# Performance work log

Measured on AMD Instinct MI355X. Metric: run time of the kernel, lower is better.

Reference implementation:

```python
import jax, jax.numpy as jnp
import numpy as np

K = 64          # tagset size (len(tag_to_ix))
START = 62      # start_tag_id
STOP = 63       # stop_tag_id
NEG = -10000.0


def setup_inputs() -> dict:
    key = jax.random.key(0)
    k1, k2, k3 = jax.random.split(key, 3)
    B, T = 1024, 512
    feats = jax.random.normal(k1, (B, T, K), dtype=jnp.float32)
    tags = jax.random.randint(k2, (B, T), 0, K, dtype=jnp.int32)
    # learned transition matrix; transitions[i, j] = score of moving from tag j to tag i
    transitions = jax.random.normal(k3, (K, K), dtype=jnp.float32)
    transitions = transitions.at[START, :].set(NEG).at[:, STOP].set(NEG)
    return {"feats": feats, "tags": tags, "transitions": transitions}


def reference(feats, tags, transitions):
    B, T, _ = feats.shape
    # log_alpha init: -10000 everywhere except start tag (matches torch code; feats[:,0] unused)
    alpha0 = jnp.full((B, K), NEG, dtype=feats.dtype).at[:, START].set(0.0)

    def step(alpha, feat_t):
        # alpha: [B, K]; new_alpha[b, i] = lse_j(transitions[i, j] + alpha[b, j]) + feat_t[b, i]
        new_alpha = jax.nn.logsumexp(transitions[None, :, :] + alpha[:, None, :], axis=-1) + feat_t
        return new_alpha, None

    feats_seq = jnp.transpose(feats[:, 1:, :], (1, 0, 2))  # [T-1, B, K]
    alpha, _ = jax.lax.scan(step, alpha0, feats_seq)
    forward_score = jax.nn.logsumexp(alpha, axis=-1)  # [B]

    # gold path score: sum_t transitions[tags[t], tags[t-1]] + feats[t, tags[t]], t = 1..T-1
    trans_score = transitions[tags[:, 1:], tags[:, :-1]].sum(axis=1)  # [B]
    emit_score = jnp.take_along_axis(feats[:, 1:, :], tags[:, 1:, None], axis=2)[..., 0].sum(axis=1)  # [B]
    gold_score = trans_score + emit_score

    return jnp.mean(forward_score - gold_score)
```

## Files before the change

kernel.cpp:

```cpp
#include <hip/hip_runtime.h>


#define BB 1024
#define TT 512
#define KK 64
#define GB 16
#define NJ 15
#define SEGLEN 32
#define LN2F 0.6931471805599453f

typedef _Float16 f16;
typedef f16   f16x8 __attribute__((ext_vector_type(8)));
typedef float f32x4 __attribute__((ext_vector_type(4)));

union W8 { f16x8 v; f16 e[8]; };

#define MFMA16(A, B, C) __builtin_amdgcn_mfma_f32_16x16x32_f16((A), (B), (C), 0, 0, 0)

__device__ __forceinline__ f32x4 exp4(f32x4 u) {
  f32x4 r; r.x = __expf(u.x); r.y = __expf(u.y); r.z = __expf(u.z); r.w = __expf(u.w);
  return r;
}

__device__ __forceinline__ unsigned umaxu(unsigned a, unsigned b) { return a > b ? a : b; }

__device__ __forceinline__ void normalize(const f32x4 (&q)[4], f32x4 (&v)[4], int& esum) {
  unsigned t0 = umaxu(umaxu(__float_as_uint(q[0].x), __float_as_uint(q[0].y)),
                      umaxu(__float_as_uint(q[0].z), __float_as_uint(q[0].w)));
  unsigned t1 = umaxu(umaxu(__float_as_uint(q[1].x), __float_as_uint(q[1].y)),
                      umaxu(__float_as_uint(q[1].z), __float_as_uint(q[1].w)));
  unsigned t2 = umaxu(umaxu(__float_as_uint(q[2].x), __float_as_uint(q[2].y)),
                      umaxu(__float_as_uint(q[2].z), __float_as_uint(q[2].w)));
  unsigned t3 = umaxu(umaxu(__float_as_uint(q[3].x), __float_as_uint(q[3].y)),
                      umaxu(__float_as_uint(q[3].z), __float_as_uint(q[3].w)));
  unsigned mb = umaxu(umaxu(t0, t1), umaxu(t2, t3));
  mb = umaxu(mb, (unsigned)__shfl_xor((int)mb, 16));
  mb = umaxu(mb, (unsigned)__shfl_xor((int)mb, 32));
  esum += (int)(mb >> 23) - 127;
  const float s = __uint_as_float(0x7F000000u - (mb & 0x7F800000u));
  #pragma unroll
  for (int tau = 0; tau < 4; ++tau) v[tau] = q[tau] * s;
}

__device__ __forceinline__ void pack_w(const f32x4 (&v)[4], W8 (&whi)[2], W8 (&wlo)[2]) {
  #pragma unroll
  for (int S = 0; S < 2; ++S) {
    #pragma unroll
    for (int c = 0; c < 2; ++c) {
      const f32x4 t = v[2 * S + c];
      const f16 h0 = (f16)t.x, h1 = (f16)t.y, h2 = (f16)t.z, h3 = (f16)t.w;
      whi[S].e[4 * c + 0] = h0;
      whi[S].e[4 * c + 1] = h1;
      whi[S].e[4 * c + 2] = h2;
      whi[S].e[4 * c + 3] = h3;
      wlo[S].e[4 * c + 0] = (f16)(t.x - (float)h0);
      wlo[S].e[4 * c + 1] = (f16)(t.y - (float)h1);
      wlo[S].e[4 * c + 2] = (f16)(t.z - (float)h2);
      wlo[S].e[4 * c + 3] = (f16)(t.w - (float)h3);
    }
  }
}

__device__ __forceinline__ void mfma_step(const W8 (&Ehi)[4][2], const W8 (&Elo)[4][2],
                                          const W8 (&whi)[2], const W8 (&wlo)[2],
                                          f32x4 (&acc)[4]) {
  #pragma unroll
  for (int tau = 0; tau < 4; ++tau) {
    f32x4 a = {0.f, 0.f, 0.f, 0.f};
    a = MFMA16(Ehi[tau][0].v, whi[0].v, a);
    a = MFMA16(Ehi[tau][1].v, whi[1].v, a);
    a = MFMA16(Elo[tau][0].v, whi[0].v, a);
    a = MFMA16(Elo[tau][1].v, whi[1].v, a);
    a = MFMA16(Ehi[tau][0].v, wlo[0].v, a);
    a = MFMA16(Ehi[tau][1].v, wlo[1].v, a);
    acc[tau] = a;
  }
}

template <int DIR, int D>
__device__ __forceinline__ void step_one(
    const float* __restrict__ fB, int j, int t_lo, int t_hi,
    const W8 (&Ehi)[4][2], const W8 (&Elo)[4][2],
    W8 (&whi)[2], W8 (&wlo)[2],
    f32x4 (&uR)[4][4], f32x4 (&g)[4],
    f32x4 (&v)[4], int& esum)
{
  f32x4 acc[4];
  mfma_step(Ehi, Elo, whi, wlo, acc);

  int tn = DIR ? (t_hi - 1 - (j + 4)) : (t_lo + (j + 4));
  if (DIR) { if (tn < t_lo) tn = t_lo; } else { if (tn > t_hi) tn = t_hi; }
  #pragma unroll
  for (int tau = 0; tau < 4; ++tau)
    uR[D][tau] = *(const f32x4*)(fB + (size_t)tn * KK + 16 * tau);

  f32x4 q[4];
  #pragma unroll
  for (int tau = 0; tau < 4; ++tau) q[tau] = acc[tau] * g[tau];
  normalize(q, v, esum);
  pack_w(v, whi, wlo);

  constexpr int DN = (D + 1) & 3;
  #pragma unroll
  for (int tau = 0; tau < 4; ++tau) g[tau] = exp4(uR[DN][tau]);
}

template <int DIR>
__device__ __forceinline__ void run_seg(
    const float* __restrict__ feats, const float* __restrict__ trans,
    int grp, int lane, int t_lo, int t_hi, int nstep, int one_hot,
    f32x4 (&v)[4], int& esum)
{
  const int m = lane & 15;
  const int h = lane >> 4;

  W8 Ehi[4][2], Elo[4][2];
  #pragma unroll
  for (int tau = 0; tau < 4; ++tau)
    #pragma unroll
    for (int S = 0; S < 2; ++S)
      #pragma unroll
      for (int e = 0; e < 8; ++e) {
        const int kk = 32 * S + 16 * (e >> 2) + 4 * h + (e & 3);
        const int row = 16 * tau + m;
        const float val = __expf(DIR ? trans[kk * KK + row] : trans[row * KK + kk]);
        const f16 hi = (f16)val;
        Ehi[tau][S].e[e] = hi;
        Elo[tau][S].e[e] = (f16)(val - (float)hi);
      }

  const float* fB = feats + (size_t)(grp * GB + m) * TT * KK + 4 * h;

  f32x4 uR[4][4];
  #pragma unroll
  for (int d = 0; d < 4; ++d) {
    int t = DIR ? (t_hi - 1 - d) : (t_lo + d);
    if (DIR) { if (t < t_lo) t = t_lo; } else { if (t > t_hi) t = t_hi; }
    #pragma unroll
    for (int tau = 0; tau < 4; ++tau)
      uR[d][tau] = *(const f32x4*)(fB + (size_t)t * KK + 16 * tau);
  }

  W8 whi[2], wlo[2];
  f32x4 g[4];
  esum = 0;

  if (DIR == 0) {
    f32x4 vv[4];
    if (one_hot) {
      #pragma unroll
      for (int tau = 0; tau < 4; ++tau) vv[tau] = (f32x4){0.f, 0.f, 0.f, 0.f};
      if (h == 3) vv[3].z = 1.0f;
    } else {
      #pragma unroll
      for (int tau = 0; tau < 4; ++tau) vv[tau] = (f32x4){1.f, 1.f, 1.f, 1.f};
    }
    pack_w(vv, whi, wlo);
  } else {
    f32x4 q[4];
    #pragma unroll
    for (int tau = 0; tau < 4; ++tau)
      q[tau] = exp4(*(const f32x4*)(fB + (size_t)t_hi * KK + 16 * tau));
    normalize(q, v, esum);
    pack_w(v, whi, wlo);
  }
  #pragma unroll
  for (int tau = 0; tau < 4; ++tau) g[tau] = exp4(uR[0][tau]);

  const int nq = nstep >> 2;
  for (int gg = 0; gg < nq; ++gg) {
    const int j = 4 * gg;
    step_one<DIR, 0>(fB, j + 0, t_lo, t_hi, Ehi, Elo, whi, wlo, uR, g, v, esum);
    step_one<DIR, 1>(fB, j + 1, t_lo, t_hi, Ehi, Elo, whi, wlo, uR, g, v, esum);
    step_one<DIR, 2>(fB, j + 2, t_lo, t_hi, Ehi, Elo, whi, wlo, uR, g, v, esum);
    step_one<DIR, 3>(fB, j + 3, t_lo, t_hi, Ehi, Elo, whi, wlo, uR, g, v, esum);
  }
  const int jr = 4 * nq;
  const int rem = nstep & 3;
  if (rem > 0) step_one<DIR, 0>(fB, jr + 0, t_lo, t_hi, Ehi, Elo, whi, wlo, uR, g, v, esum);
  if (rem > 1) step_one<DIR, 1>(fB, jr + 1, t_lo, t_hi, Ehi, Elo, whi, wlo, uR, g, v, esum);
  if (rem > 2) step_one<DIR, 2>(fB, jr + 2, t_lo, t_hi, Ehi, Elo, whi, wlo, uR, g, v, esum);

  if (DIR == 1) {
    f32x4 acc[4];
    mfma_step(Ehi, Elo, whi, wlo, acc);
    normalize(acc, v, esum);
  }
}

__global__ void zero_diff_kernel(float* __restrict__ diff) {
  diff[threadIdx.x] = 0.0f;
}

__global__ __launch_bounds__(128, 1) void crf_seg_kernel(
    const float* __restrict__ feats,
    const int*   __restrict__ tags,
    const float* __restrict__ trans,
    float*       __restrict__ diff)
{
  __shared__ float ysh[KK][GB];
  __shared__ int   esum_sh[GB];
  __shared__ float gpart[GB];

  const int chainBlocks = 64 * NJ;

  if ((int)blockIdx.x < chainBlocks) {
    const int lane = threadIdx.x & 63;
    const int wv   = threadIdx.x >> 6;
    const int grp  = blockIdx.x / NJ;
    const int j    = 1 + blockIdx.x % NJ;
    const int m = lane & 15;
    const int h = lane >> 4;

    f32x4 v[4];
    int esum;

    if (wv == 1) {
      const int t_lo = SEGLEN * j + 1;
      const int t_hi = (j == NJ) ? (TT - 1) : SEGLEN * (j + 1);
      run_seg<1>(feats, trans, grp, lane, t_lo, t_hi, t_hi - t_lo, 0, v, esum);
      #pragma unroll
      for (int tau = 0; tau < 4; ++tau) {
        ysh[16 * tau + 4 * h + 0][m] = v[tau].x;
        ysh[16 * tau + 4 * h + 1][m] = v[tau].y;
        ysh[16 * tau + 4 * h + 2][m] = v[tau].z;
        ysh[16 * tau + 4 * h + 3][m] = v[tau].w;
      }
      if (lane < 16) esum_sh[lane] = esum;
      __syncthreads();
    } else {
      const int t_lo = SEGLEN * (j - 1) + 1;
      const int t_hi = SEGLEN * j;
      run_seg<0>(feats, trans, grp, lane, t_lo, t_hi, SEGLEN, j == 1, v, esum);

      __syncthreads();

      float A = 0.f, Bs = 0.f;
      #pragma unroll
      for (int tau = 0; tau < 4; ++tau) {
        A += v[tau].x * ysh[16 * tau + 4 * h + 0][m];
        A += v[tau].y * ysh[16 * tau + 4 * h + 1][m];
        A += v[tau].z * ysh[16 * tau + 4 * h + 2][m];
        A += v[tau].w * ysh[16 * tau + 4 * h + 3][m];
        Bs += (v[tau].x + v[tau].y) + (v[tau].z + v[tau].w);
      }
      A  += __shfl_xor(A, 16);  A  += __shfl_xor(A, 32);
      Bs += __shfl_xor(Bs, 16); Bs += __shfl_xor(Bs, 32);

      if (lane < 16) {
        float c = __logf(A) + (float)(esum + esum_sh[lane]) * LN2F;
        if (j > 1) c -= __logf(Bs) + (float)esum * LN2F;
        atomicAdd(&diff[grp * GB + lane], c);
      }
    }
  } else {
    const int grp = blockIdx.x - chainBlocks;
    const int tid = threadIdx.x;
    const int m   = tid & 15;
    const int h8  = tid >> 4;
    const int bglob = grp * GB + m;
    const int* tg = tags + bglob * TT;
    const float* fg = feats + (size_t)bglob * TT * KK;

    float gs = 0.f;
    #pragma unroll 8
    for (int tt = 1 + h8; tt < TT; tt += 8) {
      const int tc = tg[tt];
      const int tp = tg[tt - 1];
      gs += trans[tc * KK + tp] + fg[(size_t)tt * KK + tc];
    }
    gs += __shfl_xor(gs, 16);
    gs += __shfl_xor(gs, 32);
    if (tid >= 64 && (tid & 63) < 16) gpart[tid & 15] = gs;
    __syncthreads();
    if (tid < 16) atomicAdd(&diff[grp * GB + tid], -(gs + gpart[tid]));
  }
}

__global__ __launch_bounds__(1024) void reduce_mean_kernel(
    const float* __restrict__ diff, float* __restrict__ out)
{
  __shared__ float part[16];
  const int tid = threadIdx.x;
  float v = diff[tid];
  #pragma unroll
  for (int off = 32; off; off >>= 1) v += __shfl_xor(v, off);
  if ((tid & 63) == 0) part[tid >> 6] = v;
  __syncthreads();
  if (tid < 16) {
    float s = part[tid];
    #pragma unroll
    for (int off = 8; off; off >>= 1) s += __shfl_xor(s, off);
    if (tid == 0) out[0] = s * (1.0f / 1024.0f);
  }
}

extern "C" void kernel_launch(void* const* d_in, const int* in_sizes, int n_in,
                              void* d_out, int out_size, void* d_ws, size_t ws_size,
                              hipStream_t stream) {
  const float* feats = (const float*)d_in[0];
  const int*   tags  = (const int*)d_in[1];
  const float* trans = (const float*)d_in[2];
  float* out  = (float*)d_out;
  float* diff = (float*)d_ws;

  zero_diff_kernel<<<dim3(1), dim3(1024), 0, stream>>>(diff);
  crf_seg_kernel<<<dim3(64 * NJ + 64), dim3(128), 0, stream>>>(feats, tags, trans, diff);
  reduce_mean_kernel<<<dim3(1), dim3(1024), 0, stream>>>(diff, out);
}
```

Baseline: 228.3 us.

## Halve segment length, precompute exp-transition MFMA fragments in a prep kernel

Splits the sequence into 31 segments of 16 steps instead of 15 of 32, doubling the number of chain blocks so the serial recurrence per block is shorter and more blocks run in parallel. The hi/lo fp16 fragments of exp(transitions) are now built once by a separate prep kernel and loaded per lane, instead of every block evaluating 64 exps per lane. Launch bounds allow up to 4 blocks per CU. This adds an extra kernel launch and more segment-combination work in exchange for a shorter critical path.

```diff
diff --git a/kernel.cpp b/kernel.cpp
--- a/kernel.cpp
+++ b/kernel.cpp
@@ -5,15 +5,15 @@
 #define TT 512
 #define KK 64
 #define GB 16
-#define NJ 15
-#define SEGLEN 32
+#define NJ 31
+#define SEGLEN 16
 #define LN2F 0.6931471805599453f
 
 typedef _Float16 f16;
 typedef f16   f16x8 __attribute__((ext_vector_type(8)));
 typedef float f32x4 __attribute__((ext_vector_type(4)));
 
-union W8 { f16x8 v; f16 e[8]; };
+union W8 { f16x8 v; f16 e[8]; uint4 u; };
 
 #define MFMA16(A, B, C) __builtin_amdgcn_mfma_f32_16x16x32_f16((A), (B), (C), 0, 0, 0)
 
@@ -107,10 +107,93 @@
 
 template <int DIR>
 __device__ __forceinline__ void run_seg(
-    const float* __restrict__ feats, const float* __restrict__ trans,
+    const float* __restrict__ feats, const uint4* __restrict__ frags,
     int grp, int lane, int t_lo, int t_hi, int nstep, int one_hot,
     f32x4 (&v)[4], int& esum)
 {
+  const int m = lane & 15;
+  const int h = lane >> 4;
+
+  W8 Ehi[4][2], Elo[4][2];
+  {
+    const uint4* fr = frags + DIR * 1024 + lane;
+    #pragma unroll
+    for (int tau = 0; tau < 4; ++tau)
+      #pragma unroll
+      for (int S = 0; S < 2; ++S) {
+        Ehi[tau][S].u = fr[(tau * 2 + S) * 64];
+        Elo[tau][S].u = fr[(8 + tau * 2 + S) * 64];
+      }
+  }
+
+  const float* fB = feats + (size_t)(grp * GB + m) * TT * KK + 4 * h;
+
+  f32x4 uR[4][4];
+  #pragma unroll
+  for (int d = 0; d < 4; ++d) {
+    int t = DIR ? (t_hi - 1 - d) : (t_lo + d);
+    if (DIR) { if (t < t_lo) t = t_lo; } else { if (t > t_hi) t = t_hi; }
+    #pragma unroll
+    for (int tau = 0; tau < 4; ++tau)
+      uR[d][tau] = *(const f32x4*)(fB + (size_t)t * KK + 16 * tau);
+  }
+
+  W8 whi[2], wlo[2];
+  f32x4 g[4];
+  esum = 0;
+
+  if (DIR == 0) {
+    f32x4 vv[4];
+    if (one_hot) {
+      #pragma unroll
+      for (int tau = 0; tau < 4; ++tau) vv[tau] = (f32x4){0.f, 0.f, 0.f, 0.f};
+      if (h == 3) vv[3].z = 1.0f;
+    } else {
+      #pragma unroll
+      for (int tau = 0; tau < 4; ++tau) vv[tau] = (f32x4){1.f, 1.f, 1.f, 1.f};
+    }
+    pack_w(vv, whi, wlo);
+  } else {
+    f32x4 q[4];
+    #pragma unroll
+    for (int tau = 0; tau < 4; ++tau)
+      q[tau] = exp4(*(const f32x4*)(fB + (size_t)t_hi * KK + 16 * tau));
+    normalize(q, v, esum);
+    pack_w(v, whi, wlo);
+  }
+  #pragma unroll
+  for (int tau = 0; tau < 4; ++tau) g[tau] = exp4(uR[0][tau]);
+
+  const int nq = nstep >> 2;
+  for (int gg = 0; gg < nq; ++gg) {
+    const int j = 4 * gg;
+    step_one<DIR, 0>(fB, j + 0, t_lo, t_hi, Ehi, Elo, whi, wlo, uR, g, v, esum);
+    step_one<DIR, 1>(fB, j + 1, t_lo, t_hi, Ehi, Elo, whi, wlo, uR, g, v, esum);
+    step_one<DIR, 2>(fB, j + 2, t_lo, t_hi, Ehi, Elo, whi, wlo, uR, g, v, esum);
+    step_one<DIR, 3>(fB, j + 3, t_lo, t_hi, Ehi, Elo, whi, wlo, uR, g, v, esum);
+  }
+  const int jr = 4 * nq;
+  const int rem = nstep & 3;
+  if (rem > 0) step_one<DIR, 0>(fB, jr + 0, t_lo, t_hi, Ehi, Elo, whi, wlo, uR, g, v, esum);
+  if (rem > 1) step_one<DIR, 1>(fB, jr + 1, t_lo, t_hi, Ehi, Elo, whi, wlo, uR, g, v, esum);
+  if (rem > 2) step_one<DIR, 2>(fB, jr + 2, t_lo, t_hi, Ehi, Elo, whi, wlo, uR, g, v, esum);
+
+  if (DIR == 1) {
+    f32x4 acc[4];
+    mfma_step(Ehi, Elo, whi, wlo, acc);
+    normalize(acc, v, esum);
+  }
+}
+
+__global__ void zero_diff_kernel(float* __restrict__ diff) {
+  diff[threadIdx.x] = 0.0f;
+}
+
+__global__ __launch_bounds__(128) void prep_kernel(
+    const float* __restrict__ trans, uint4* __restrict__ frags)
+{
+  const int lane = threadIdx.x & 63;
+  const int DIR  = threadIdx.x >> 6;
   const int m = lane & 15;
   const int h = lane >> 4;
 
@@ -129,73 +212,21 @@
         Elo[tau][S].e[e] = (f16)(val - (float)hi);
       }
 
-  const float* fB = feats + (size_t)(grp * GB + m) * TT * KK + 4 * h;
-
-  f32x4 uR[4][4];
-  #pragma unroll
-  for (int d = 0; d < 4; ++d) {
-    int t = DIR ? (t_hi - 1 - d) : (t_lo + d);
-    if (DIR) { if (t < t_lo) t = t_lo; } else { if (t > t_hi) t = t_hi; }
-    #pragma unroll
-    for (int tau = 0; tau < 4; ++tau)
-      uR[d][tau] = *(const f32x4*)(fB + (size_t)t * KK + 16 * tau);
-  }
-
-  W8 whi[2], wlo[2];
-  f32x4 g[4];
-  esum = 0;
-
-  if (DIR == 0) {
-    f32x4 vv[4];
-    if (one_hot) {
-      #pragma unroll
-      for (int tau = 0; tau < 4; ++tau) vv[tau] = (f32x4){0.f, 0.f, 0.f, 0.f};
-      if (h == 3) vv[3].z = 1.0f;
-    } else {
-      #pragma unroll
-      for (int tau = 0; tau < 4; ++tau) vv[tau] = (f32x4){1.f, 1.f, 1.f, 1.f};
-    }
-    pack_w(vv, whi, wlo);
-  } else {
-    f32x4 q[4];
-    #pragma unroll
-    for (int tau = 0; tau < 4; ++tau)
-      q[tau] = exp4(*(const f32x4*)(fB + (size_t)t_hi * KK + 16 * tau));
-    normalize(q, v, esum);
-    pack_w(v, whi, wlo);
-  }
-  #pragma unroll
-  for (int tau = 0; tau < 4; ++tau) g[tau] = exp4(uR[0][tau]);
-
-  const int nq = nstep >> 2;
-  for (int gg = 0; gg < nq; ++gg) {
-    const int j = 4 * gg;
-    step_one<DIR, 0>(fB, j + 0, t_lo, t_hi, Ehi, Elo, whi, wlo, uR, g, v, esum);
-    step_one<DIR, 1>(fB, j + 1, t_lo, t_hi, Ehi, Elo, whi, wlo, uR, g, v, esum);
-    step_one<DIR, 2>(fB, j + 2, t_lo, t_hi, Ehi, Elo, whi, wlo, uR, g, v, esum);
-    step_one<DIR, 3>(fB, j + 3, t_lo, t_hi, Ehi, Elo, whi, wlo, uR, g, v, esum);
-  }
-  const int jr = 4 * nq;
-  const int rem = nstep & 3;
-  if (rem > 0) step_one<DIR, 0>(fB, jr + 0, t_lo, t_hi, Ehi, Elo, whi, wlo, uR, g, v, esum);
-  if (rem > 1) step_one<DIR, 1>(fB, jr + 1, t_lo, t_hi, Ehi, Elo, whi, wlo, uR, g, v, esum);
-  if (rem > 2) step_one<DIR, 2>(fB, jr + 2, t_lo, t_hi, Ehi, Elo, whi, wlo, uR, g, v, esum);
-
-  if (DIR == 1) {
-    f32x4 acc[4];
-    mfma_step(Ehi, Elo, whi, wlo, acc);
-    normalize(acc, v, esum);
-  }
-}
-
-__global__ void zero_diff_kernel(float* __restrict__ diff) {
-  diff[threadIdx.x] = 0.0f;
-}
-
-__global__ __launch_bounds__(128, 1) void crf_seg_kernel(
+  uint4* fr = frags + DIR * 1024 + lane;
+  #pragma unroll
+  for (int tau = 0; tau < 4; ++tau)
+    #pragma unroll
+    for (int S = 0; S < 2; ++S) {
+      fr[(tau * 2 + S) * 64]     = Ehi[tau][S].u;
+      fr[(8 + tau * 2 + S) * 64] = Elo[tau][S].u;
+    }
+}
+
+__global__ __launch_bounds__(128, 4) void crf_seg_kernel(
     const float* __restrict__ feats,
     const int*   __restrict__ tags,
     const float* __restrict__ trans,
+    const uint4* __restrict__ frags,
     float*       __restrict__ diff)
 {
   __shared__ float ysh[KK][GB];
@@ -218,7 +249,7 @@
     if (wv == 1) {
       const int t_lo = SEGLEN * j + 1;
       const int t_hi = (j == NJ) ? (TT - 1) : SEGLEN * (j + 1);
-      run_seg<1>(feats, trans, grp, lane, t_lo, t_hi, t_hi - t_lo, 0, v, esum);
+      run_seg<1>(feats, frags, grp, lane, t_lo, t_hi, t_hi - t_lo, 0, v, esum);
       #pragma unroll
       for (int tau = 0; tau < 4; ++tau) {
         ysh[16 * tau + 4 * h + 0][m] = v[tau].x;
@@ -231,7 +262,7 @@
     } else {
       const int t_lo = SEGLEN * (j - 1) + 1;
       const int t_hi = SEGLEN * j;
-      run_seg<0>(feats, trans, grp, lane, t_lo, t_hi, SEGLEN, j == 1, v, esum);
+      run_seg<0>(feats, frags, grp, lane, t_lo, t_hi, SEGLEN, j == 1, v, esum);
 
       __syncthreads();
 
@@ -303,8 +334,10 @@
   const float* trans = (const float*)d_in[2];
   float* out  = (float*)d_out;
   float* diff = (float*)d_ws;
+  uint4* frags = (uint4*)((char*)d_ws + 4096);
 
   zero_diff_kernel<<<dim3(1), dim3(1024), 0, stream>>>(diff);
-  crf_seg_kernel<<<dim3(64 * NJ + 64), dim3(128), 0, stream>>>(feats, tags, trans, diff);
+  prep_kernel<<<dim3(1), dim3(128), 0, stream>>>(trans, frags);
+  crf_seg_kernel<<<dim3(64 * NJ + 64), dim3(128), 0, stream>>>(feats, tags, trans, frags, diff);
   reduce_mean_kernel<<<dim3(1), dim3(1024), 0, stream>>>(diff, out);
 }
```

New measurement: 322.9 us. 1.41x slower.
